# Kernel tuning notes

Measured on AMD Instinct MI355X. Metric: run time of the kernel, lower is better.

The kernel has to match this reference:

```python
import jax, jax.numpy as jnp
import numpy as np

KSIZE = 11
SIGMA = 1.5
PAD = KSIZE // 2
C1 = 0.01 ** 2
C2 = 0.03 ** 2


def gaussian_kernel(ksize, sigma):
    ax = np.arange(ksize, dtype=np.float32) - (ksize - 1) / 2.0
    g = np.exp(-(ax ** 2) / (2.0 * sigma ** 2))
    k2d = np.outer(g, g)
    k2d = k2d / k2d.sum()
    # depthwise kernel for 3 channels: [out=3, in/groups=1, kh, kw]
    return jnp.asarray(np.broadcast_to(k2d, (3, 1, ksize, ksize)).copy())


def dwconv(x, kernel):
    # x: [B,3,H,W], kernel: [3,1,k,k], 'same' padding, groups=3
    return jax.lax.conv_general_dilated(
        x, kernel,
        window_strides=(1, 1),
        padding=[(PAD, PAD), (PAD, PAD)],
        dimension_numbers=('NCHW', 'OIHW', 'NCHW'),
        feature_group_count=3)


def setup_inputs() -> dict:
    key = jax.random.key(0)
    k1, k2 = jax.random.split(key)
    shape = (16, 3, 512, 512)
    img_output = jax.random.uniform(k1, shape, dtype=jnp.float32)
    img_target = jax.random.uniform(k2, shape, dtype=jnp.float32)
    kernel = gaussian_kernel(KSIZE, SIGMA)
    return {"img_output": img_output, "img_target": img_target, "kernel": kernel}


def reference(img_output, img_target, kernel):
    s, t = img_output, img_target
    ux = dwconv(s, kernel)
    uy = dwconv(t, kernel)
    uxx = dwconv(s * s, kernel)
    uyy = dwconv(t * t, kernel)
    uxy = dwconv(s * t, kernel)
    ssim = ((2 * ux * uy + C1) * (2 * (uxy - ux * uy) + C2)
            / (ux ** 2 + uy ** 2 + C1)
            / (uxx - ux * ux + (uyy - uy * uy) + C2))
    return 1.0 - ssim.mean()
```

## Files before the change

kernel.cpp:

```cpp
#include <hip/hip_runtime.h>

typedef _Float16 f16;
typedef f16  f16x8 __attribute__((ext_vector_type(8)));
typedef f16  f16x4 __attribute__((ext_vector_type(4)));
typedef f16  f16x2 __attribute__((ext_vector_type(2)));
typedef float f32x4 __attribute__((ext_vector_type(4)));

#define W 512
#define H 512
#define KS 11
#define NW 4
#define NBLK 3072
#define NLINES 256
#define C1_SSIM 0.0001f
#define C2_SSIM 0.0009f
#define NTOTAL 12582912.0f

#define LROWS 80
#define LSTRIDE 80

__device__ __constant__ const float GW[KS] = {
    1.02838e-3f, 7.59876e-3f, 3.600076e-2f, 1.0936069e-1f, 2.1300554e-1f,
    2.6601172e-1f,
    2.1300554e-1f, 1.0936069e-1f, 3.600076e-2f, 7.59876e-3f, 1.02838e-3f
};

__device__ inline float ssim_px(float ux, float uy, float uxx, float uyy, float uxy) {
    const float uxuy = ux * uy;
    const float a = 2.f * uxuy + C1_SSIM;
    const float b = 2.f * (uxy - uxuy) + C2_SSIM;
    const float c = ux * ux + uy * uy + C1_SSIM;
    const float d = (uxx - ux * ux) + (uyy - uy * uy) + C2_SSIM;
    return (a * b) * __builtin_amdgcn_rcpf(c * d);
}

struct __attribute__((aligned(16))) F4 { float x, y, z, w; };

__device__ __forceinline__ f16x8 pack8(const float v[8]) {
    f16x8 r;
    #pragma unroll
    for (int p = 0; p < 4; ++p) {
        const f16x2 h = __builtin_bit_cast(
            f16x2, __builtin_amdgcn_cvt_pkrtz(v[2 * p], v[2 * p + 1]));
        r[2 * p]     = h[0];
        r[2 * p + 1] = h[1];
    }
    return r;
}

__global__ __launch_bounds__(256, 6)
void ssim_main(const float* __restrict__ simg, const float* __restrict__ timg,
               float* __restrict__ accum) {
    __shared__ __align__(16) f16 lds[2][LROWS * LSTRIDE];
    __shared__ float red[NW];

    const int tid  = threadIdx.x;
    const int w    = tid >> 6;
    const int lane = tid & 63;
    const int n    = lane & 15;
    const int q    = lane >> 4;

    const int bid = blockIdx.x;
    const int z   = bid >> 6;
    const int rr  = bid & 63;
    const int ty  = rr >> 3;
    const int tx  = rr & 7;

    const float* sp = simg + ((size_t)z << 18);
    const float* tp = timg + ((size_t)z << 18);
    const int x0    = tx << 6;
    const int ybase = (ty << 6) - 5;
    const int xbase = x0 - 8;

    #pragma unroll
    for (int it = 0; it < 7; ++it) {
        const int t = it * 256 + tid;
        if (it < 6 || t < 1600) {
            const int img = (t >= 800) ? 1 : 0;
            const int u   = img ? (t - 800) : t;
            const int lr  = (u * 205) >> 11;
            const int sg  = u - lr * 10;
            const int ry  = ybase + lr;
            const int cx  = xbase + (sg << 3);
            const float* src = img ? tp : sp;
            float v[8];
            const bool ok = ((unsigned)ry < (unsigned)H) &
                            ((unsigned)cx <= (unsigned)(W - 8));
            if (ok) {
                const float* rp = src + ((size_t)ry << 9) + cx;
                const F4 a = *(const F4*)rp;
                const F4 b = *(const F4*)(rp + 4);
                v[0] = a.x; v[1] = a.y; v[2] = a.z; v[3] = a.w;
                v[4] = b.x; v[5] = b.y; v[6] = b.z; v[7] = b.w;
            } else {
                #pragma unroll
                for (int j = 0; j < 8; ++j) v[j] = 0.f;
            }
            *(f16x8*)&lds[img][lr * LSTRIDE + (sg << 3)] = pack8(v);
        }
    }

    f16x8 af;
    #pragma unroll
    for (int j = 0; j < 8; ++j) {
        const int k = (q << 3) + j;
        const int d = k - n - 3;
        af[j] = (d >= 0 && d < KS) ? (f16)GW[d] : (f16)0.f;
    }
    f16x4 a1v, a2v;
    #pragma unroll
    for (int j = 0; j < 4; ++j) {
        const int k  = (q << 2) + j;
        const int d1 = k - n;
        const int d2 = k + 16 - n;
        a1v[j] = (d1 >= 0 && d1 < KS) ? (f16)GW[d1] : (f16)0.f;
        a2v[j] = (d2 >= 0 && d2 < KS) ? (f16)GW[d2] : (f16)0.f;
    }

    __syncthreads();

    union H4 { f16x4 v4; f16x2 v2[2]; };
    const int coff = (w << 4) + (q << 3);
    const f16* lss = &lds[0][coff];
    const f16* lts = &lds[1][coff];

    f16x4 ph[2][5];
    float sum = 0.f;

    #pragma unroll
    for (int g = 0; g < 5; ++g) {
        const int rowoff = ((g << 4) + n) * LSTRIDE;
        const f16x8 sf = *(const f16x8*)(lss + rowoff);
        const f16x8 tf = *(const f16x8*)(lts + rowoff);
        const int pb = g & 1;
        #pragma unroll
        for (int c = 0; c < 5; ++c) {
            f16x8 ch;
            if      (c == 0) ch = sf;
            else if (c == 1) ch = tf;
            else if (c == 2) ch = sf * sf;
            else if (c == 3) ch = tf * tf;
            else             ch = sf * tf;
            const f32x4 zero = {0.f, 0.f, 0.f, 0.f};
            const f32x4 d = __builtin_amdgcn_mfma_f32_16x16x32_f16(ch, af, zero, 0, 0, 0);
            H4 u;
            u.v2[0] = __builtin_bit_cast(f16x2, __builtin_amdgcn_cvt_pkrtz(d[0], d[1]));
            u.v2[1] = __builtin_bit_cast(f16x2, __builtin_amdgcn_cvt_pkrtz(d[2], d[3]));
            ph[pb][c] = u.v4;
        }
        if (g >= 1) {
            const int pa = pb ^ 1;
            f32x4 acc[5];
            #pragma unroll
            for (int c = 0; c < 5; ++c) {
                const f32x4 zero = {0.f, 0.f, 0.f, 0.f};
                f32x4 a = __builtin_amdgcn_mfma_f32_16x16x16f16(a2v, ph[pb][c], zero, 0, 0, 0);
                a = __builtin_amdgcn_mfma_f32_16x16x16f16(a1v, ph[pa][c], a, 0, 0, 0);
                acc[c] = a;
            }
            #pragma unroll
            for (int rg = 0; rg < 4; ++rg)
                sum += ssim_px(acc[0][rg], acc[1][rg], acc[2][rg],
                               acc[3][rg], acc[4][rg]);
        }
    }

    #pragma unroll
    for (int off = 32; off > 0; off >>= 1)
        sum += __shfl_down(sum, off, 64);
    if (lane == 0) red[w] = sum;
    __syncthreads();
    if (tid == 0) {
        atomicAdd(&accum[(blockIdx.x & (NLINES - 1)) << 4],
                  red[0] + red[1] + red[2] + red[3]);
    }
}

__global__ void ssim_final(const float* __restrict__ accum, float* __restrict__ out) {
    const int lane = threadIdx.x;
    float s = 0.f;
    #pragma unroll
    for (int i = 0; i < NLINES / 64; ++i)
        s += accum[((i << 6) + lane) << 4];
    #pragma unroll
    for (int off = 32; off > 0; off >>= 1)
        s += __shfl_down(s, off, 64);
    if (lane == 0) out[0] = 1.f - s * (1.f / NTOTAL);
}

extern "C" void kernel_launch(void* const* d_in, const int* in_sizes, int n_in,
                              void* d_out, int out_size, void* d_ws, size_t ws_size,
                              hipStream_t stream) {
    const float* s = (const float*)d_in[0];
    const float* t = (const float*)d_in[1];
    float* out   = (float*)d_out;
    float* accum = (float*)d_ws;

    hipMemsetAsync(accum, 0, NLINES * 16 * sizeof(float), stream);
    ssim_main<<<dim3(NBLK), 256, 0, stream>>>(s, t, accum);
    ssim_final<<<1, 64, 0, stream>>>(accum, out);
}
```

Before: 139.1 us.

## Load input tiles directly into LDS via global_load_lds as fp32

Replaces the register-staged global loads plus fp16 packing with direct global-to-LDS DMA loads of 16 bytes per lane, storing fp32 tiles in LDS and converting to fp16 when reading for MFMA. Out-of-bounds pieces are sourced from a zeroed workspace buffer. This removes VGPR traffic and conversion work from the load phase but doubles LDS footprint and lowers the occupancy target from 6 to 3 blocks per CU, reducing latency hiding.

After: 138.5 us. About the same (-0.5%).

```diff
diff --git a/kernel.cpp b/kernel.cpp
--- a/kernel.cpp
+++ b/kernel.cpp
@@ -1,4 +1,5 @@
 #include <hip/hip_runtime.h>
+#include <stdint.h>
 
 typedef _Float16 f16;
 typedef f16  f16x8 __attribute__((ext_vector_type(8)));
@@ -17,7 +18,8 @@
 #define NTOTAL 12582912.0f
 
 #define LROWS 80
-#define LSTRIDE 80
+#define LCOLS 80
+#define NCHUNK 50
 
 __device__ __constant__ const float GW[KS] = {
     1.02838e-3f, 7.59876e-3f, 3.600076e-2f, 1.0936069e-1f, 2.1300554e-1f,
@@ -34,24 +36,24 @@
     return (a * b) * __builtin_amdgcn_rcpf(c * d);
 }
 
-struct __attribute__((aligned(16))) F4 { float x, y, z, w; };
-
-__device__ __forceinline__ f16x8 pack8(const float v[8]) {
+__device__ __forceinline__ f16x8 pack84(f32x4 a, f32x4 b) {
     f16x8 r;
-    #pragma unroll
-    for (int p = 0; p < 4; ++p) {
-        const f16x2 h = __builtin_bit_cast(
-            f16x2, __builtin_amdgcn_cvt_pkrtz(v[2 * p], v[2 * p + 1]));
-        r[2 * p]     = h[0];
-        r[2 * p + 1] = h[1];
-    }
+    f16x2 h;
+    h = __builtin_bit_cast(f16x2, __builtin_amdgcn_cvt_pkrtz(a[0], a[1]));
+    r[0] = h[0]; r[1] = h[1];
+    h = __builtin_bit_cast(f16x2, __builtin_amdgcn_cvt_pkrtz(a[2], a[3]));
+    r[2] = h[0]; r[3] = h[1];
+    h = __builtin_bit_cast(f16x2, __builtin_amdgcn_cvt_pkrtz(b[0], b[1]));
+    r[4] = h[0]; r[5] = h[1];
+    h = __builtin_bit_cast(f16x2, __builtin_amdgcn_cvt_pkrtz(b[2], b[3]));
+    r[6] = h[0]; r[7] = h[1];
     return r;
 }
 
-__global__ __launch_bounds__(256, 6)
+__global__ __launch_bounds__(256, 3)
 void ssim_main(const float* __restrict__ simg, const float* __restrict__ timg,
-               float* __restrict__ accum) {
-    __shared__ __align__(16) f16 lds[2][LROWS * LSTRIDE];
+               float* __restrict__ accum, const float* __restrict__ zbuf) {
+    __shared__ __align__(16) float lds[2][LROWS * LCOLS];
     __shared__ float red[NW];
 
     const int tid  = threadIdx.x;
@@ -73,30 +75,26 @@
     const int xbase = x0 - 8;
 
     #pragma unroll
-    for (int it = 0; it < 7; ++it) {
-        const int t = it * 256 + tid;
-        if (it < 6 || t < 1600) {
-            const int img = (t >= 800) ? 1 : 0;
-            const int u   = img ? (t - 800) : t;
-            const int lr  = (u * 205) >> 11;
-            const int sg  = u - lr * 10;
-            const int ry  = ybase + lr;
-            const int cx  = xbase + (sg << 3);
+    for (int k = 0; k < 13; ++k) {
+        const int c = (k << 2) + w;
+        if (c < NCHUNK) {
+            const int img  = (c >= 25) ? 1 : 0;
+            const int cc   = img ? (c - 25) : c;
+            const int off  = (cc << 10) + (lane << 4);
+            const int t    = off >> 6;
+            const int row  = (t * 205) >> 10;
+            const int colb = off - row * 320;
+            const int ry   = ybase + row;
+            const int gcol = xbase + (colb >> 2);
             const float* src = img ? tp : sp;
-            float v[8];
             const bool ok = ((unsigned)ry < (unsigned)H) &
-                            ((unsigned)cx <= (unsigned)(W - 8));
-            if (ok) {
-                const float* rp = src + ((size_t)ry << 9) + cx;
-                const F4 a = *(const F4*)rp;
-                const F4 b = *(const F4*)(rp + 4);
-                v[0] = a.x; v[1] = a.y; v[2] = a.z; v[3] = a.w;
-                v[4] = b.x; v[5] = b.y; v[6] = b.z; v[7] = b.w;
-            } else {
-                #pragma unroll
-                for (int j = 0; j < 8; ++j) v[j] = 0.f;
-            }
-            *(f16x8*)&lds[img][lr * LSTRIDE + (sg << 3)] = pack8(v);
+                            ((unsigned)gcol <= (unsigned)(W - 4));
+            const float* ga = ok ? (src + ((size_t)ry << 9) + gcol) : zbuf;
+            void* ldst = (char*)(&lds[0][0]) + (c << 10);
+            __builtin_amdgcn_global_load_lds(
+                (const uint32_t __attribute__((address_space(1)))*)ga,
+                (uint32_t __attribute__((address_space(3)))*)ldst,
+                16, 0, 0);
         }
     }
 
@@ -121,17 +119,21 @@
 
     union H4 { f16x4 v4; f16x2 v2[2]; };
     const int coff = (w << 4) + (q << 3);
-    const f16* lss = &lds[0][coff];
-    const f16* lts = &lds[1][coff];
+    const float* ls = &lds[0][coff];
+    const float* lt = &lds[1][coff];
 
     f16x4 ph[2][5];
     float sum = 0.f;
 
     #pragma unroll
     for (int g = 0; g < 5; ++g) {
-        const int rowoff = ((g << 4) + n) * LSTRIDE;
-        const f16x8 sf = *(const f16x8*)(lss + rowoff);
-        const f16x8 tf = *(const f16x8*)(lts + rowoff);
+        const int ro = ((g << 4) + n) * LCOLS;
+        const f32x4 s0 = *(const f32x4*)(ls + ro);
+        const f32x4 s1 = *(const f32x4*)(ls + ro + 4);
+        const f32x4 t0 = *(const f32x4*)(lt + ro);
+        const f32x4 t1 = *(const f32x4*)(lt + ro + 4);
+        const f16x8 sf = pack84(s0, s1);
+        const f16x8 tf = pack84(t0, t1);
         const int pb = g & 1;
         #pragma unroll
         for (int c = 0; c < 5; ++c) {
@@ -195,8 +197,9 @@
     const float* t = (const float*)d_in[1];
     float* out   = (float*)d_out;
     float* accum = (float*)d_ws;
-
-    hipMemsetAsync(accum, 0, NLINES * 16 * sizeof(float), stream);
-    ssim_main<<<dim3(NBLK), 256, 0, stream>>>(s, t, accum);
+    const float* zbuf = accum + NLINES * 16;
+
+    hipMemsetAsync(accum, 0, NLINES * 16 * sizeof(float) + 256, stream);
+    ssim_main<<<dim3(NBLK), 256, 0, stream>>>(s, t, accum, zbuf);
     ssim_final<<<1, 64, 0, stream>>>(accum, out);
 }
```

## Halve tile height, remap blocks across XCDs, fuse final reduction via last-block

Applied to the files above, without the earlier changes.

Tiles shrink from 64x64 to 32 rows by 64 columns, doubling the block count and cutting LDS per block so more blocks fit per CU (launch bounds raised to 8). Block IDs are permuted so consecutive logical tiles are spread across the eight XCDs. The separate finalize kernel is removed: a global counter selects the last block, which sums the partial accumulators and writes the output. The cost is a larger vertical halo overhead (10 of 42 rows loaded per tile) and an extra atomic and fence per block.

Result: slower. 300.7 us (+116.2%).

```diff
diff --git a/kernel.cpp b/kernel.cpp
--- a/kernel.cpp
+++ b/kernel.cpp
@@ -1,4 +1,5 @@
 #include <hip/hip_runtime.h>
+#include <stdint.h>
 
 typedef _Float16 f16;
 typedef f16  f16x8 __attribute__((ext_vector_type(8)));
@@ -10,14 +11,14 @@
 #define H 512
 #define KS 11
 #define NW 4
-#define NBLK 3072
+#define NBLK 6144
 #define NLINES 256
 #define C1_SSIM 0.0001f
 #define C2_SSIM 0.0009f
 #define NTOTAL 12582912.0f
 
-#define LROWS 80
 #define LSTRIDE 80
+#define IMGF16 3840
 
 __device__ __constant__ const float GW[KS] = {
     1.02838e-3f, 7.59876e-3f, 3.600076e-2f, 1.0936069e-1f, 2.1300554e-1f,
@@ -48,11 +49,26 @@
     return r;
 }
 
-__global__ __launch_bounds__(256, 6)
+__device__ __forceinline__ void load8f(const float* __restrict__ base, int ry,
+                                       int xs, float v[8]) {
+    if ((unsigned)ry < (unsigned)H && (unsigned)xs <= (unsigned)(W - 8)) {
+        const float* r = base + ((size_t)ry << 9) + xs;
+        const F4 a = *(const F4*)r;
+        const F4 b = *(const F4*)(r + 4);
+        v[0] = a.x; v[1] = a.y; v[2] = a.z; v[3] = a.w;
+        v[4] = b.x; v[5] = b.y; v[6] = b.z; v[7] = b.w;
+    } else {
+        #pragma unroll
+        for (int j = 0; j < 8; ++j) v[j] = 0.f;
+    }
+}
+
+__global__ __launch_bounds__(256, 8)
 void ssim_main(const float* __restrict__ simg, const float* __restrict__ timg,
-               float* __restrict__ accum) {
-    __shared__ __align__(16) f16 lds[2][LROWS * LSTRIDE];
+               float* __restrict__ ws, float* __restrict__ out) {
+    __shared__ __align__(16) f16 lds[2][IMGF16];
     __shared__ float red[NW];
+    __shared__ int lastflag;
 
     const int tid  = threadIdx.x;
     const int w    = tid >> 6;
@@ -61,41 +77,27 @@
     const int q    = lane >> 4;
 
     const int bid = blockIdx.x;
-    const int z   = bid >> 6;
-    const int rr  = bid & 63;
+    const int L   = (bid & 7) * (NBLK / 8) + (bid >> 3);
+    const int z   = L >> 7;
+    const int rr  = L & 127;
     const int ty  = rr >> 3;
     const int tx  = rr & 7;
 
     const float* sp = simg + ((size_t)z << 18);
     const float* tp = timg + ((size_t)z << 18);
-    const int x0    = tx << 6;
-    const int ybase = (ty << 6) - 5;
-    const int xbase = x0 - 8;
-
-    #pragma unroll
-    for (int it = 0; it < 7; ++it) {
-        const int t = it * 256 + tid;
-        if (it < 6 || t < 1600) {
-            const int img = (t >= 800) ? 1 : 0;
-            const int u   = img ? (t - 800) : t;
-            const int lr  = (u * 205) >> 11;
-            const int sg  = u - lr * 10;
-            const int ry  = ybase + lr;
-            const int cx  = xbase + (sg << 3);
-            const float* src = img ? tp : sp;
+    const int ybase = (ty << 5) - 5;
+    const int xbase = (tx << 6) - 8;
+
+    #pragma unroll
+    for (int it = 0; it < 4; ++it) {
+        const int u = (it << 8) + tid;
+        if (it < 3 || u < 960) {
+            const int img = (u >= 480) ? 1 : 0;
+            const int uu  = img ? (u - 480) : u;
+            const int lr  = (uu * 205) >> 11;
+            const int sg  = uu - lr * 10;
             float v[8];
-            const bool ok = ((unsigned)ry < (unsigned)H) &
-                            ((unsigned)cx <= (unsigned)(W - 8));
-            if (ok) {
-                const float* rp = src + ((size_t)ry << 9) + cx;
-                const F4 a = *(const F4*)rp;
-                const F4 b = *(const F4*)(rp + 4);
-                v[0] = a.x; v[1] = a.y; v[2] = a.z; v[3] = a.w;
-                v[4] = b.x; v[5] = b.y; v[6] = b.z; v[7] = b.w;
-            } else {
-                #pragma unroll
-                for (int j = 0; j < 8; ++j) v[j] = 0.f;
-            }
+            load8f(img ? tp : sp, ybase + lr, xbase + (sg << 3), v);
             *(f16x8*)&lds[img][lr * LSTRIDE + (sg << 3)] = pack8(v);
         }
     }
@@ -128,10 +130,10 @@
     float sum = 0.f;
 
     #pragma unroll
-    for (int g = 0; g < 5; ++g) {
-        const int rowoff = ((g << 4) + n) * LSTRIDE;
-        const f16x8 sf = *(const f16x8*)(lss + rowoff);
-        const f16x8 tf = *(const f16x8*)(lts + rowoff);
+    for (int g = 0; g < 3; ++g) {
+        const int ro = ((g << 4) + n) * LSTRIDE;
+        const f16x8 sf = *(const f16x8*)(lss + ro);
+        const f16x8 tf = *(const f16x8*)(lts + ro);
         const int pb = g & 1;
         #pragma unroll
         for (int c = 0; c < 5; ++c) {
@@ -171,21 +173,24 @@
     if (lane == 0) red[w] = sum;
     __syncthreads();
     if (tid == 0) {
-        atomicAdd(&accum[(blockIdx.x & (NLINES - 1)) << 4],
+        atomicAdd(&ws[(bid & (NLINES - 1)) << 4],
                   red[0] + red[1] + red[2] + red[3]);
-    }
-}
-
-__global__ void ssim_final(const float* __restrict__ accum, float* __restrict__ out) {
-    const int lane = threadIdx.x;
-    float s = 0.f;
-    #pragma unroll
-    for (int i = 0; i < NLINES / 64; ++i)
-        s += accum[((i << 6) + lane) << 4];
-    #pragma unroll
-    for (int off = 32; off > 0; off >>= 1)
-        s += __shfl_down(s, off, 64);
-    if (lane == 0) out[0] = 1.f - s * (1.f / NTOTAL);
+        __threadfence();
+        const unsigned old = atomicAdd((unsigned*)(ws + (NLINES << 4)), 1u);
+        lastflag = (old == (unsigned)(NBLK - 1));
+    }
+    __syncthreads();
+    if (lastflag) {
+        __threadfence();
+        float s = atomicAdd(&ws[tid << 4], 0.f);
+        #pragma unroll
+        for (int off = 32; off > 0; off >>= 1)
+            s += __shfl_down(s, off, 64);
+        if (lane == 0) red[w] = s;
+        __syncthreads();
+        if (tid == 0)
+            out[0] = 1.f - (red[0] + red[1] + red[2] + red[3]) * (1.f / NTOTAL);
+    }
 }
 
 extern "C" void kernel_launch(void* const* d_in, const int* in_sizes, int n_in,
@@ -193,10 +198,9 @@
                               hipStream_t stream) {
     const float* s = (const float*)d_in[0];
     const float* t = (const float*)d_in[1];
-    float* out   = (float*)d_out;
-    float* accum = (float*)d_ws;
-
-    hipMemsetAsync(accum, 0, NLINES * 16 * sizeof(float), stream);
-    ssim_main<<<dim3(NBLK), 256, 0, stream>>>(s, t, accum);
-    ssim_final<<<1, 64, 0, stream>>>(accum, out);
-}
+    float* out = (float*)d_out;
+    float* ws  = (float*)d_ws;
+
+    hipMemsetAsync(ws, 0, (NLINES * 16 + 16) * sizeof(float), stream);
+    ssim_main<<<dim3(NBLK), 256, 0, stream>>>(s, t, ws, out);
+}
```
